# Kernel optimization log

Hardware: AMD Instinct MI355X
Metric: run time of the kernel (lower is better)

## Reference

```python
import jax, jax.numpy as jnp
import numpy as np
import math

NUM_EXPERTS = 8
MIN_EXPERTS_ACTIVE = 2  # max(1, 8 // 4) per __init__ formula


def setup_inputs() -> dict:
    key = jax.random.key(0)
    ks = jax.random.split(key, 6)
    N, Cin, H, W = 16384, 68, 8, 8
    Cproj = 128
    patch = jax.random.normal(ks[0], (N, Cin, H, W), dtype=jnp.float32)
    conv_w = jax.random.normal(ks[1], (Cproj, Cin, 3, 3), dtype=jnp.float32) * (1.0 / np.sqrt(Cin * 9))
    conv_b = jnp.zeros((Cproj,), dtype=jnp.float32)
    fc_w = jax.random.normal(ks[2], (Cproj, NUM_EXPERTS), dtype=jnp.float32) * (1.0 / np.sqrt(Cproj))
    fc_b = jnp.zeros((NUM_EXPERTS,), dtype=jnp.float32)
    wth_max_c = jnp.float32(0.4)
    wth_entropy_c = jnp.float32(0.3)
    wth_gap_c = jnp.float32(0.3)
    threshold = jnp.float32(0.2)
    return {
        'patch': patch, 'conv_w': conv_w, 'conv_b': conv_b,
        'fc_w': fc_w, 'fc_b': fc_b,
        'wth_max_c': wth_max_c, 'wth_entropy_c': wth_entropy_c, 'wth_gap_c': wth_gap_c,
        'threshold': threshold, 'layer_idx': 0, 'current_epoch': 30,
    }


def _gate(patch, conv_w, conv_b, fc_w, fc_b):
    # 3x3 SAME conv (NCHW) -> ReLU -> global avg pool -> linear
    y = jax.lax.conv_general_dilated(
        patch, conv_w, window_strides=(1, 1), padding='SAME',
        dimension_numbers=('NCHW', 'OIHW', 'NCHW'))
    y = jax.nn.relu(y + conv_b[None, :, None, None])
    pooled = y.mean(axis=(2, 3))  # [N, Cproj]
    return pooled @ fc_w + fc_b   # [N, E]


def _compute_gap(sw):
    # sw: [N, E] sorted descending
    k = min(4, NUM_EXPERTS - 1)
    mean_rest = sw[:, 1:k + 1].mean(axis=-1, keepdims=True)
    gap = (sw[:, 0:1] - mean_rest) / (sw[:, 0:1] + 1e-8)
    return jnp.clip(gap, 0.0, 1.0)


def _adaptive_threshold(w, base_threshold, wth_max_c, wth_entropy_c, wth_gap_c):
    sw = -jnp.sort(-w, axis=-1)  # descending
    max_component = 1.0 - sw[:, 0:1]
    mean_w = w.mean(axis=-1, keepdims=True)
    std_w = w.std(axis=-1, keepdims=True, ddof=1)  # torch default unbiased
    entropy = -(w * jnp.log(w + 1e-18)).sum(axis=-1, keepdims=True)
    entropy_component = 1.0 - entropy / math.log(NUM_EXPERTS)
    gap_component = _compute_gap(sw)
    adaptive_factor = (wth_max_c * max_component + wth_entropy_c * entropy_component
                       + wth_gap_c * gap_component)
    th = base_threshold * (0.5 + adaptive_factor)
    min_th = jnp.maximum(jnp.float32(0.05), mean_w - 0.5 * std_w)
    max_th = jnp.minimum(jnp.float32(0.7), sw[:, 0:1] - 0.1 * std_w)
    th = jnp.clip(th, min_th, max_th)
    kth = sw[:, MIN_EXPERTS_ACTIVE - 1:MIN_EXPERTS_ACTIVE]
    return jnp.minimum(th, kth * 0.9)


def reference(patch, conv_w, conv_b, fc_w, fc_b,
              wth_max_c, wth_entropy_c, wth_gap_c,
              threshold, layer_idx, current_epoch):
    logits = _gate(patch, conv_w, conv_b, fc_w, fc_b)
    weights = jax.nn.softmax(logits, axis=-1)
    th = _adaptive_threshold(weights, threshold, wth_max_c, wth_entropy_c, wth_gap_c)
    if current_epoch is not None and current_epoch < 20:
        weights_norm = jnp.ones_like(weights) / NUM_EXPERTS
    elif current_epoch is not None and 20 <= current_epoch <= 25:
        tau = max(0.1, 1.0 - (current_epoch - 20) * 0.18)
        s = jax.nn.sigmoid((weights - th) / tau)
        weights_norm = s / jnp.clip(s.sum(axis=-1, keepdims=True), 1e-8)
    else:  # current_epoch > 25 or eval: straight-through hard/soft masking
        tau = 0.1
        hard = (weights > th).astype(weights.dtype)
        soft = jax.nn.sigmoid((weights - th) / tau)
        filtered = hard + jax.lax.stop_gradient(soft - hard)
        weights_norm = filtered / jnp.clip(filtered.sum(axis=-1, keepdims=True), 1e-8)
    return weights_norm
```

## Files before the change

### kernel.cpp

```cpp
#include <hip/hip_runtime.h>


typedef _Float16 half8 __attribute__((ext_vector_type(8)));
typedef float    floatx4 __attribute__((ext_vector_type(4)));

#define LDS_A_SAMPLE 9216
#define LDS_B_OFF    36864
#define LDS_P_OFF    (36864 + 8192)
#define LDS_TOTAL    (36864 + 8192 + 2048)

__global__ void prep_weights(const float* __restrict__ cw, _Float16* __restrict__ Bw) {
  int i = blockIdx.x * 256 + threadIdx.x;
  int co = i / 672;
  int k  = i - co * 672;
  int s  = k / 72;
  int ci = k - s * 72;
  float v = 0.f;
  if (s < 9 && ci < 68) {
    int ky = s / 3, kx = s - 3 * ky;
    v = cw[((co * 68 + ci) * 3 + ky) * 3 + kx];
  }
  Bw[i] = (_Float16)v;
}

__global__ __launch_bounds__(256, 2) void router_main(
    const float* __restrict__ patch,
    const float* __restrict__ conv_b,
    const _Float16* __restrict__ Bw,
    const float* __restrict__ fc_w,
    const float* __restrict__ fc_b,
    const float* __restrict__ p_wmax,
    const float* __restrict__ p_went,
    const float* __restrict__ p_wgap,
    const float* __restrict__ p_thr,
    const int* __restrict__ p_epoch,
    float* __restrict__ out)
{
  __shared__ __align__(16) unsigned char lds[LDS_TOTAL];
  const int tid    = threadIdx.x;
  const int l      = tid & 63;
  const int w      = tid >> 6;
  const int lane15 = l & 15;
  const int quad   = l >> 4;
  const int m_half = w >> 1;
  const int n0     = (w & 1) * 64;
  const int n_s    = blockIdx.x * 4;

  {
    const float* psrc = patch + (size_t)(n_s + w) * 4352 + l;
    unsigned char* arow = lds + w * LDS_A_SAMPLE + l * 144;
    #pragma unroll
    for (int b = 0; b < 9; ++b) {
      half8 h;
      #pragma unroll
      for (int j = 0; j < 8; ++j) {
        int ci = b * 8 + j;
        float v = (ci < 68) ? psrc[ci * 64] : 0.f;
        h[j] = (_Float16)v;
      }
      *(half8*)(arow + b * 16) = h;
    }
  }

  const int bco   = tid >> 1;
  const int bhalf = tid & 1;
  {
    const float4* src = (const float4*)(Bw + bco * 672 + bhalf * 16);
    float4 r0 = src[0], r1 = src[1];
    *(float4*)(lds + LDS_B_OFF + tid * 32)      = r0;
    *(float4*)(lds + LDS_B_OFF + tid * 32 + 16) = r1;
  }
  __syncthreads();

  floatx4 acc[8][4];
  floatx4 zacc = {0.f, 0.f, 0.f, 0.f};
  #pragma unroll
  for (int t = 0; t < 8; ++t)
    #pragma unroll
    for (int n = 0; n < 4; ++n) acc[t][n] = zacc;

  half8 zz;
  #pragma unroll
  for (int j = 0; j < 8; ++j) zz[j] = (_Float16)0.f;

  for (int c = 0; c < 21; ++c) {
    float4 pf0, pf1;
    if (c < 20) {
      const float4* src = (const float4*)(Bw + bco * 672 + (c + 1) * 32 + bhalf * 16);
      pf0 = src[0]; pf1 = src[1];
    }
    int kb  = c * 4 + quad;
    int s   = (kb * 57) >> 9;
    int ci0 = (kb - s * 9) * 8;
    int dy  = (s * 11) >> 5;
    int dx  = s - 3 * dy;
    bool kval = (kb < 81);

    half8 afr[8];
    #pragma unroll
    for (int t = 0; t < 8; ++t) {
      int p = (t & 3) * 16 + lane15;
      int y = p >> 3, x = p & 7;
      int sy = y + dy - 1, sx = x + dx - 1;
      bool v = kval && (sy >= 0) && (sy < 8) && (sx >= 0) && (sx < 8);
      int q = v ? (sy * 8 + sx) : 0;
      int g = m_half * 2 + (t >> 2);
      afr[t] = *(const half8*)(lds + g * LDS_A_SAMPLE + q * 144 + ci0 * 2);
      afr[t] = v ? afr[t] : zz;
    }
    half8 bfr[4];
    #pragma unroll
    for (int n = 0; n < 4; ++n) {
      int co = n0 + n * 16 + lane15;
      bfr[n] = *(const half8*)(lds + LDS_B_OFF + co * 64 + quad * 16);
    }
    #pragma unroll
    for (int t = 0; t < 8; ++t)
      #pragma unroll
      for (int n = 0; n < 4; ++n)
        acc[t][n] = __builtin_amdgcn_mfma_f32_16x16x32_f16(afr[t], bfr[n], acc[t][n], 0, 0, 0);

    if (c < 20) {
      __syncthreads();
      *(float4*)(lds + LDS_B_OFF + tid * 32)      = pf0;
      *(float4*)(lds + LDS_B_OFF + tid * 32 + 16) = pf1;
      __syncthreads();
    }
  }

  float bcoef[4];
  #pragma unroll
  for (int n = 0; n < 4; ++n) bcoef[n] = conv_b[n0 + n * 16 + lane15];

  float* pl = (float*)(lds + LDS_P_OFF);
  #pragma unroll
  for (int gl = 0; gl < 2; ++gl) {
    #pragma unroll
    for (int n = 0; n < 4; ++n) {
      float ssum = 0.f;
      #pragma unroll
      for (int tt = 0; tt < 4; ++tt) {
        int t = gl * 4 + tt;
        #pragma unroll
        for (int r = 0; r < 4; ++r)
          ssum += fmaxf(acc[t][n][r] + bcoef[n], 0.f);
      }
      ssum += __shfl_xor(ssum, 16);
      ssum += __shfl_xor(ssum, 32);
      if (l < 16) {
        int g = m_half * 2 + gl;
        pl[g * 128 + n0 + n * 16 + lane15] = ssum * (1.f / 64.f);
      }
    }
  }
  __syncthreads();

  const float* plw = pl + w * 128;
  int e  = l >> 3;
  int c8 = l & 7;
  float part = 0.f;
  #pragma unroll
  for (int m = 0; m < 16; ++m) {
    int co = c8 + 8 * m;
    part += plw[co] * fc_w[co * 8 + e];
  }
  part += __shfl_xor(part, 1);
  part += __shfl_xor(part, 2);
  part += __shfl_xor(part, 4);

  float lg[8];
  #pragma unroll
  for (int j = 0; j < 8; ++j) lg[j] = __shfl(part, j * 8) + fc_b[j];

  float mx = lg[0];
  #pragma unroll
  for (int j = 1; j < 8; ++j) mx = fmaxf(mx, lg[j]);
  float wgt[8]; float sum = 0.f;
  #pragma unroll
  for (int j = 0; j < 8; ++j) { wgt[j] = expf(lg[j] - mx); sum += wgt[j]; }
  float inv = 1.f / sum;
  #pragma unroll
  for (int j = 0; j < 8; ++j) wgt[j] *= inv;

  float sw[8];
  #pragma unroll
  for (int j = 0; j < 8; ++j) sw[j] = wgt[j];
  #define CSD(i, j) { float hi_ = fmaxf(sw[i], sw[j]); float lo_ = fminf(sw[i], sw[j]); sw[i] = hi_; sw[j] = lo_; }
  CSD(0,1) CSD(2,3) CSD(4,5) CSD(6,7)
  CSD(0,2) CSD(1,3) CSD(4,6) CSD(5,7)
  CSD(1,2) CSD(5,6)
  CSD(0,4) CSD(1,5) CSD(2,6) CSD(3,7)
  CSD(2,4) CSD(3,5)
  CSD(1,2) CSD(3,4) CSD(5,6)
  #undef CSD

  float s1 = 0.f;
  #pragma unroll
  for (int j = 0; j < 8; ++j) s1 += wgt[j];
  float mean = s1 * 0.125f;
  float var = 0.f;
  #pragma unroll
  for (int j = 0; j < 8; ++j) { float d = wgt[j] - mean; var += d * d; }
  float stdv = sqrtf(var * (1.f / 7.f));
  float ent = 0.f;
  #pragma unroll
  for (int j = 0; j < 8; ++j) ent -= wgt[j] * logf(wgt[j] + 1e-18f);

  float maxc  = 1.f - sw[0];
  float entc  = 1.f - ent * 0.48089834696298783f;
  float mrest = (sw[1] + sw[2] + sw[3] + sw[4]) * 0.25f;
  float gap   = (sw[0] - mrest) / (sw[0] + 1e-8f);
  gap = fminf(fmaxf(gap, 0.f), 1.f);
  float af = p_wmax[0] * maxc + p_went[0] * entc + p_wgap[0] * gap;
  float th = p_thr[0] * (0.5f + af);
  float mn  = fmaxf(0.05f, mean - 0.5f * stdv);
  float mxt = fminf(0.7f, sw[0] - 0.1f * stdv);
  th = fminf(fmaxf(th, mn), mxt);
  th = fminf(th, sw[1] * 0.9f);

  int epoch = p_epoch[0];
  float outv[8];
  if (epoch < 20) {
    #pragma unroll
    for (int j = 0; j < 8; ++j) outv[j] = 0.125f;
  } else {
    float tau = (epoch <= 25) ? fmaxf(0.1f, 1.0f - (float)(epoch - 20) * 0.18f) : 0.1f;
    float ssum = 0.f;
    #pragma unroll
    for (int j = 0; j < 8; ++j) {
      float sj = 1.f / (1.f + expf(-(wgt[j] - th) / tau));
      outv[j] = sj; ssum += sj;
    }
    float invs = 1.f / fmaxf(ssum, 1e-8f);
    #pragma unroll
    for (int j = 0; j < 8; ++j) outv[j] *= invs;
  }

  if (l < 8) {
    float mv = outv[0];
    #pragma unroll
    for (int j = 1; j < 8; ++j) mv = (l == j) ? outv[j] : mv;
    out[(n_s + w) * 8 + l] = mv;
  }
}

extern "C" void kernel_launch(void* const* d_in, const int* in_sizes, int n_in,
                              void* d_out, int out_size, void* d_ws, size_t ws_size,
                              hipStream_t stream) {
  const float* patch  = (const float*)d_in[0];
  const float* conv_w = (const float*)d_in[1];
  const float* conv_b = (const float*)d_in[2];
  const float* fc_w   = (const float*)d_in[3];
  const float* fc_b   = (const float*)d_in[4];
  const float* wmax   = (const float*)d_in[5];
  const float* went   = (const float*)d_in[6];
  const float* wgap   = (const float*)d_in[7];
  const float* thr    = (const float*)d_in[8];
  const int*   epoch  = (const int*)d_in[10];
  float* outp = (float*)d_out;
  _Float16* Bw = (_Float16*)d_ws;

  int N = in_sizes[0] / 4352;
  prep_weights<<<336, 256, 0, stream>>>(conv_w, Bw);
  router_main<<<N / 4, 256, 0, stream>>>(patch, conv_b, Bw, fc_w, fc_b,
                                         wmax, went, wgap, thr, epoch, outp);
}
```

Before: 518.2 us.

## Zero-pad input halo in LDS and stream conv weights from global into registers

The per-sample input tile in LDS becomes a zero-initialised 10x10 padded layout, so im2col fragment loads need no bounds checks or select masks and use precomputed base offsets. Conv weight fragments are now loaded straight from global memory (L2-resident) into registers with one-step-ahead prefetch, replacing the LDS staging buffer and the two block barriers per K-chunk. The final K-chunk is peeled, relying on the zero padding in the prepared weights for the out-of-range lanes. In exchange, LDS use per block grows and every wave issues its own global weight loads instead of sharing one staged copy.

```diff
diff --git a/kernel.cpp b/kernel.cpp
--- a/kernel.cpp
+++ b/kernel.cpp
@@ -4,10 +4,9 @@
 typedef _Float16 half8 __attribute__((ext_vector_type(8)));
 typedef float    floatx4 __attribute__((ext_vector_type(4)));
 
-#define LDS_A_SAMPLE 9216
-#define LDS_B_OFF    36864
-#define LDS_P_OFF    (36864 + 8192)
-#define LDS_TOTAL    (36864 + 8192 + 2048)
+#define A_SAMPLE  14400
+#define LDS_P_OFF 57600
+#define LDS_TOTAL 59648
 
 __global__ void prep_weights(const float* __restrict__ cw, _Float16* __restrict__ Bw) {
   int i = blockIdx.x * 256 + threadIdx.x;
@@ -47,8 +46,18 @@
   const int n_s    = blockIdx.x * 4;
 
   {
+    unsigned char* abase = lds + w * A_SAMPLE;
+    float4 z4 = make_float4(0.f, 0.f, 0.f, 0.f);
+    #pragma unroll
+    for (int j = 0; j < 15; ++j) {
+      int idx = j * 64 + l;
+      if (idx < 900) *(float4*)(abase + idx * 16) = z4;
+    }
+  }
+  {
     const float* psrc = patch + (size_t)(n_s + w) * 4352 + l;
-    unsigned char* arow = lds + w * LDS_A_SAMPLE + l * 144;
+    int y = l >> 3, x = l & 7;
+    unsigned char* arow = lds + w * A_SAMPLE + ((y + 1) * 10 + (x + 1)) * 144;
     #pragma unroll
     for (int b = 0; b < 9; ++b) {
       half8 h;
@@ -61,16 +70,20 @@
       *(half8*)(arow + b * 16) = h;
     }
   }
-
-  const int bco   = tid >> 1;
-  const int bhalf = tid & 1;
-  {
-    const float4* src = (const float4*)(Bw + bco * 672 + bhalf * 16);
-    float4 r0 = src[0], r1 = src[1];
-    *(float4*)(lds + LDS_B_OFF + tid * 32)      = r0;
-    *(float4*)(lds + LDS_B_OFF + tid * 32 + 16) = r1;
-  }
   __syncthreads();
+
+  int apos[8];
+  #pragma unroll
+  for (int t = 0; t < 8; ++t) {
+    int p  = (t & 3) * 16 + lane15;
+    int pp = ((p >> 3) + 1) * 10 + (p & 7) + 1;
+    apos[t] = (m_half * 2 + (t >> 2)) * A_SAMPLE + pp * 144;
+  }
+
+  const _Float16* bptr[4];
+  #pragma unroll
+  for (int n = 0; n < 4; ++n)
+    bptr[n] = Bw + (size_t)(n0 + n * 16 + lane15) * 672 + quad * 8;
 
   floatx4 acc[8][4];
   floatx4 zacc = {0.f, 0.f, 0.f, 0.f};
@@ -79,53 +92,50 @@
     #pragma unroll
     for (int n = 0; n < 4; ++n) acc[t][n] = zacc;
 
-  half8 zz;
-  #pragma unroll
-  for (int j = 0; j < 8; ++j) zz[j] = (_Float16)0.f;
-
-  for (int c = 0; c < 21; ++c) {
-    float4 pf0, pf1;
-    if (c < 20) {
-      const float4* src = (const float4*)(Bw + bco * 672 + (c + 1) * 32 + bhalf * 16);
-      pf0 = src[0]; pf1 = src[1];
-    }
+  half8 bcur[4];
+  #pragma unroll
+  for (int n = 0; n < 4; ++n) bcur[n] = *(const half8*)(bptr[n]);
+
+  #pragma unroll 4
+  for (int c = 0; c < 20; ++c) {
+    half8 bnext[4];
+    #pragma unroll
+    for (int n = 0; n < 4; ++n)
+      bnext[n] = *(const half8*)(bptr[n] + (c + 1) * 32);
+
     int kb  = c * 4 + quad;
     int s   = (kb * 57) >> 9;
-    int ci0 = (kb - s * 9) * 8;
+    int rem = kb - s * 9;
     int dy  = (s * 11) >> 5;
     int dx  = s - 3 * dy;
-    bool kval = (kb < 81);
+    int roff = (dy * 10 + dx - 11) * 144 + rem * 16;
 
     half8 afr[8];
     #pragma unroll
-    for (int t = 0; t < 8; ++t) {
-      int p = (t & 3) * 16 + lane15;
-      int y = p >> 3, x = p & 7;
-      int sy = y + dy - 1, sx = x + dx - 1;
-      bool v = kval && (sy >= 0) && (sy < 8) && (sx >= 0) && (sx < 8);
-      int q = v ? (sy * 8 + sx) : 0;
-      int g = m_half * 2 + (t >> 2);
-      afr[t] = *(const half8*)(lds + g * LDS_A_SAMPLE + q * 144 + ci0 * 2);
-      afr[t] = v ? afr[t] : zz;
-    }
-    half8 bfr[4];
-    #pragma unroll
-    for (int n = 0; n < 4; ++n) {
-      int co = n0 + n * 16 + lane15;
-      bfr[n] = *(const half8*)(lds + LDS_B_OFF + co * 64 + quad * 16);
-    }
+    for (int t = 0; t < 8; ++t)
+      afr[t] = *(const half8*)(lds + apos[t] + roff);
+
     #pragma unroll
     for (int t = 0; t < 8; ++t)
       #pragma unroll
       for (int n = 0; n < 4; ++n)
-        acc[t][n] = __builtin_amdgcn_mfma_f32_16x16x32_f16(afr[t], bfr[n], acc[t][n], 0, 0, 0);
-
-    if (c < 20) {
-      __syncthreads();
-      *(float4*)(lds + LDS_B_OFF + tid * 32)      = pf0;
-      *(float4*)(lds + LDS_B_OFF + tid * 32 + 16) = pf1;
-      __syncthreads();
-    }
+        acc[t][n] = __builtin_amdgcn_mfma_f32_16x16x32_f16(afr[t], bcur[n], acc[t][n], 0, 0, 0);
+
+    #pragma unroll
+    for (int n = 0; n < 4; ++n) bcur[n] = bnext[n];
+  }
+
+  {
+    int roff = (quad == 0) ? 1712 : 0;
+    half8 afr[8];
+    #pragma unroll
+    for (int t = 0; t < 8; ++t)
+      afr[t] = *(const half8*)(lds + apos[t] + roff);
+    #pragma unroll
+    for (int t = 0; t < 8; ++t)
+      #pragma unroll
+      for (int n = 0; n < 4; ++n)
+        acc[t][n] = __builtin_amdgcn_mfma_f32_16x16x32_f16(afr[t], bcur[n], acc[t][n], 0, 0, 0);
   }
 
   float bcoef[4];
```

Measured after the change: 496.2 us. 4.3% less time.
